# Optimization experiments

Measured on AMD Instinct MI355X. Metric: run time of the kernel, lower is better.

## Reference

```python
import jax, jax.numpy as jnp
import numpy as np

N_NODES = 50000
N_EDGES = 800000
D_FEAT = 128
D_EDGE = 64
N_HEADS = 4
OUT_DIM = 32
HID = N_HEADS * OUT_DIM  # 128


def segment_softmax(logits, seg, num_segments):
    # jraph.segment_softmax: subtract per-segment max, exp, normalize by per-segment sum
    seg_max = jax.ops.segment_max(logits, seg, num_segments=num_segments)
    e = jnp.exp(logits - seg_max[seg])
    denom = jax.ops.segment_sum(e, seg, num_segments=num_segments)
    return e / denom[seg]


def setup_inputs() -> dict:
    key = jax.random.key(0)
    ks = jax.random.split(key, 12)
    s = 1.0 / np.sqrt(D_FEAT)
    se = 1.0 / np.sqrt(D_EDGE)
    return {
        "nodes": jax.random.normal(ks[0], (N_NODES, D_FEAT), jnp.float32),
        "edges": jax.random.normal(ks[1], (N_EDGES, D_EDGE), jnp.float32),
        "senders": jax.random.randint(ks[2], (N_EDGES,), 0, N_NODES, jnp.int32),
        "receivers": jax.random.randint(ks[3], (N_EDGES,), 0, N_NODES, jnp.int32),
        "Wq": jax.random.normal(ks[4], (D_FEAT, HID), jnp.float32) * s,
        "bq": jnp.zeros((HID,), jnp.float32),
        "Wk": jax.random.normal(ks[5], (D_FEAT, HID), jnp.float32) * s,
        "bk": jnp.zeros((HID,), jnp.float32),
        "Wv": jax.random.normal(ks[6], (D_FEAT, HID), jnp.float32) * s,
        "bv": jnp.zeros((HID,), jnp.float32),
        "We": jax.random.normal(ks[7], (D_EDGE, HID), jnp.float32) * se,
        "Wu": jax.random.normal(ks[8], (D_FEAT, OUT_DIM), jnp.float32) * s,
        "bu": jnp.zeros((OUT_DIM,), jnp.float32),
    }


def reference(nodes, edges, senders, receivers, Wq, bq, Wk, bk, Wv, bv, We, Wu, bu):
    n_nodes = nodes.shape[0]
    send_feats = nodes[senders]    # [E, D]
    recv_feats = nodes[receivers]  # [E, D]

    q = (recv_feats @ Wq + bq).reshape(-1, N_HEADS, OUT_DIM)
    k = (send_feats @ Wk + bk).reshape(-1, N_HEADS, OUT_DIM)
    v = (send_feats @ Wv + bv).reshape(-1, N_HEADS, OUT_DIM)
    e = (edges @ We).reshape(-1, N_HEADS, OUT_DIM)

    attn = (q * k).sum(-1) / jnp.sqrt(jnp.asarray(OUT_DIM, q.dtype))  # [E, H]
    attn = segment_softmax(attn, receivers, n_nodes)                  # [E, H]

    msgs = (attn[:, :, None] * (v + e)).mean(axis=1)                  # [E, OUT_DIM]
    aggr = jax.ops.segment_sum(msgs, receivers, num_segments=n_nodes) # [N, OUT_DIM]

    feats = nodes @ Wu + bu
    return jax.nn.relu(feats + aggr)
```

## Files before the change

### kernel.cpp

```cpp
#include <hip/hip_runtime.h>
#include <math.h>

#define N_NODES 50000
#define N_EDGES 800000
#define D_FEAT 128
#define D_EDGE 64
#define HID 128
#define OUT_DIM 32

typedef unsigned short u16;
typedef short bf16x8 __attribute__((ext_vector_type(8)));
typedef float f32x4 __attribute__((ext_vector_type(4)));

__device__ __forceinline__ u16 f2bf(float x) {
    unsigned u = __float_as_uint(x);
    unsigned r = (u >> 16) & 1u;
    return (u16)((u + 0x7FFFu + r) >> 16);
}
__device__ __forceinline__ float bf2f(u16 s) { return __uint_as_float(((unsigned)s) << 16); }
__device__ __forceinline__ float bflo(unsigned u) { return __uint_as_float(u << 16); }
__device__ __forceinline__ float bfhi(unsigned u) { return __uint_as_float(u & 0xFFFF0000u); }

__global__ void zero_i32(int* __restrict__ p, int n) {
    int i = blockIdx.x * 256 + threadIdx.x;
    if (i < n) p[i] = 0;
}

__global__ void prep_WeT(const float* __restrict__ We, u16* __restrict__ WeTg) {
    int id = blockIdx.x * 256 + threadIdx.x;
    int c = id >> 6, k = id & 63;
    WeTg[c * 64 + k] = f2bf(We[k * HID + c]);
}

__global__ __launch_bounds__(256) void node_qkv_gemm2b(
    const float* __restrict__ nodes,
    const float* __restrict__ Wq, const float* __restrict__ bq,
    const float* __restrict__ Wk, const float* __restrict__ bk,
    const float* __restrict__ Wv, const float* __restrict__ bv,
    u16* __restrict__ Q, u16* __restrict__ Kk, u16* __restrict__ V)
{
    const int c0 = blockIdx.y * 64;
    const int n0 = blockIdx.x * 64;
    const float* Ws[3] = {Wq, Wk, Wv};
    const float* bs[3] = {bq, bk, bv};
    u16* Cs[3]         = {Q, Kk, V};

    __shared__ float Alds[32][68];
    __shared__ float Wlds[3][32][64];

    const int tid = threadIdx.x;
    const int tx = tid & 15, ty = tid >> 4;
    const int r = ty * 4, c = tx * 4;
    float acc[3][4][4] = {};

    for (int kk = 0; kk < D_FEAT; kk += 32) {
        #pragma unroll
        for (int it = 0; it < 2; ++it) {
            int idx = tid + it * 256;
            int an = idx >> 3;
            int ak = (idx & 7) * 4;
            float4 v4 = make_float4(0.f, 0.f, 0.f, 0.f);
            if (n0 + an < N_NODES)
                v4 = *(const float4*)&nodes[(size_t)(n0 + an) * D_FEAT + kk + ak];
            Alds[ak + 0][an] = v4.x;
            Alds[ak + 1][an] = v4.y;
            Alds[ak + 2][an] = v4.z;
            Alds[ak + 3][an] = v4.w;
        }
        #pragma unroll
        for (int it = 0; it < 6; ++it) {
            int idx = tid + it * 256;
            int m  = idx >> 9;
            int rm = idx & 511;
            int wk = rm >> 4;
            int wc = (rm & 15) * 4;
            *(float4*)&Wlds[m][wk][wc] = *(const float4*)&Ws[m][(size_t)(kk + wk) * HID + c0 + wc];
        }
        __syncthreads();
        #pragma unroll
        for (int k = 0; k < 32; ++k) {
            float4 a4 = *(const float4*)&Alds[k][r];
            float av[4] = {a4.x, a4.y, a4.z, a4.w};
            #pragma unroll
            for (int m = 0; m < 3; ++m) {
                float4 w4 = *(const float4*)&Wlds[m][k][c];
                float wv[4] = {w4.x, w4.y, w4.z, w4.w};
                #pragma unroll
                for (int i = 0; i < 4; ++i)
                    #pragma unroll
                    for (int j = 0; j < 4; ++j)
                        acc[m][i][j] += av[i] * wv[j];
            }
        }
        __syncthreads();
    }
    #pragma unroll
    for (int m = 0; m < 3; ++m) {
        #pragma unroll
        for (int i = 0; i < 4; ++i) {
            int n = n0 + r + i;
            if (n < N_NODES) {
                ushort4 o;
                o.x = f2bf(acc[m][i][0] + bs[m][c0 + c + 0]);
                o.y = f2bf(acc[m][i][1] + bs[m][c0 + c + 1]);
                o.z = f2bf(acc[m][i][2] + bs[m][c0 + c + 2]);
                o.w = f2bf(acc[m][i][3] + bs[m][c0 + c + 3]);
                *(ushort4*)&Cs[m][(size_t)n * HID + c0 + c] = o;
            }
        }
    }
}

__global__ void hist_kernel(const int* __restrict__ receivers, int* __restrict__ count) {
    int e = blockIdx.x * 256 + threadIdx.x;
    atomicAdd(&count[receivers[e]], 1);
}

__global__ __launch_bounds__(256) void scan1(const int* __restrict__ count,
                                             int* __restrict__ incl, int* __restrict__ bsum) {
    __shared__ int sh[256];
    int gid = blockIdx.x * 256 + threadIdx.x;
    int v = (gid < N_NODES) ? count[gid] : 0;
    sh[threadIdx.x] = v; __syncthreads();
    #pragma unroll
    for (int off = 1; off < 256; off <<= 1) {
        int t = (threadIdx.x >= off) ? sh[threadIdx.x - off] : 0;
        __syncthreads();
        sh[threadIdx.x] += t;
        __syncthreads();
    }
    if (gid < N_NODES) incl[gid] = sh[threadIdx.x];
    if (threadIdx.x == 255) bsum[blockIdx.x] = sh[255];
}

__global__ __launch_bounds__(256) void scan2(const int* __restrict__ bsum,
                                             int* __restrict__ boff, int nblocks) {
    __shared__ int sh[256];
    int v = (threadIdx.x < nblocks) ? bsum[threadIdx.x] : 0;
    sh[threadIdx.x] = v; __syncthreads();
    #pragma unroll
    for (int off = 1; off < 256; off <<= 1) {
        int t = (threadIdx.x >= off) ? sh[threadIdx.x - off] : 0;
        __syncthreads();
        sh[threadIdx.x] += t;
        __syncthreads();
    }
    boff[threadIdx.x] = sh[threadIdx.x] - v;
}

__global__ __launch_bounds__(256) void scan3(const int* __restrict__ incl,
                                             const int* __restrict__ count,
                                             const int* __restrict__ boff,
                                             int* __restrict__ startp, int* __restrict__ cursor) {
    int gid = blockIdx.x * 256 + threadIdx.x;
    if (gid < N_NODES) {
        int ex = incl[gid] - count[gid] + boff[blockIdx.x];
        startp[gid] = ex;
        cursor[gid] = ex;
    }
    if (gid == 0) startp[N_NODES] = N_EDGES;
}

__global__ void scatter_kernel(const int* __restrict__ receivers,
                               int* __restrict__ cursor, int* __restrict__ sorted,
                               int* __restrict__ epos) {
    int e = blockIdx.x * 256 + threadIdx.x;
    int r = receivers[e];
    int pos = atomicAdd(&cursor[r], 1);
    sorted[pos] = e;
    epos[e] = pos;
}

__global__ __launch_bounds__(256) void edge_logits_sorted_b(
    const u16* __restrict__ Q, const u16* __restrict__ K,
    const int* __restrict__ senders, const int* __restrict__ receivers,
    const int* __restrict__ sorted, float* __restrict__ wbuf)
{
    int id = blockIdx.x * 256 + threadIdx.x;
    int i = id >> 2, h = id & 3;
    int e = sorted[i];
    int s = senders[e], r = receivers[e];
    const uint4* qp = (const uint4*)&Q[(size_t)r * HID + h * 32];
    const uint4* kp = (const uint4*)&K[(size_t)s * HID + h * 32];
    float acc = 0.f;
    #pragma unroll
    for (int j = 0; j < 4; ++j) {
        uint4 a = qp[j], b = kp[j];
        acc += bflo(a.x) * bflo(b.x) + bfhi(a.x) * bfhi(b.x);
        acc += bflo(a.y) * bflo(b.y) + bfhi(a.y) * bfhi(b.y);
        acc += bflo(a.z) * bflo(b.z) + bfhi(a.z) * bfhi(b.z);
        acc += bflo(a.w) * bflo(b.w) + bfhi(a.w) * bfhi(b.w);
    }
    wbuf[id] = expf(acc * 0.17677669529663687f);
}

__global__ __launch_bounds__(256) void denom_norm(
    const int* __restrict__ startp, float* __restrict__ wbuf)
{
    int id = blockIdx.x * 256 + threadIdx.x;
    if (id >= N_NODES * 4) return;
    int n = id >> 2, h = id & 3;
    int s = startp[n], e = startp[n + 1];
    float acc = 0.f;
    for (int i = s; i < e; ++i)
        acc += wbuf[(size_t)i * 4 + h];
    float inv = 0.25f / acc;
    for (int i = s; i < e; ++i)
        wbuf[(size_t)i * 4 + h] *= inv;
}

__global__ __launch_bounds__(256, 2) void edge_messages_v5(
    const float* __restrict__ edges, const u16* __restrict__ WeTg,
    const u16* __restrict__ V, const float* __restrict__ wbuf,
    const int* __restrict__ senders, const int* __restrict__ epos,
    u16* __restrict__ msg)
{
    __shared__ __align__(16) u16 smem[18432];
    u16* Ae  = smem;
    u16* WeT = smem + 9216;
    u16* Ep  = smem;

    const int tid = threadIdx.x;
    const int e0 = blockIdx.x * 128;

    const int eloc = tid >> 1, half = tid & 1;
    const int eg = e0 + eloc;
    const int snd = senders[eg];
    const int pos = epos[eg];
    const float4 w4 = *(const float4*)&wbuf[(size_t)pos * 4];
    const float wA = half ? w4.z : w4.x;
    const float wB = half ? w4.w : w4.y;
    uint4 vv[8];
    {
        const uint4* vp = (const uint4*)&V[(size_t)snd * HID + half * 64];
        #pragma unroll
        for (int i = 0; i < 8; ++i) vv[i] = vp[i];
    }

    #pragma unroll
    for (int it = 0; it < 8; ++it) {
        int idx = tid + it * 256;
        int e  = idx >> 4;
        int k4 = (idx & 15) * 4;
        float4 v = *(const float4*)&edges[(size_t)(e0 + e) * D_EDGE + k4];
        ushort4 b;
        b.x = f2bf(v.x); b.y = f2bf(v.y); b.z = f2bf(v.z); b.w = f2bf(v.w);
        *(ushort4*)&Ae[e * 72 + k4] = b;
    }
    {
        int c = tid >> 1, part = tid & 1;
        const uint4* src = (const uint4*)&WeTg[c * 64 + part * 32];
        uint4* dst = (uint4*)&WeT[c * 72 + part * 32];
        dst[0] = src[0];
        dst[1] = src[1];
        dst[2] = src[2];
        dst[3] = src[3];
    }
    __syncthreads();

    const int wave = tid >> 6, lane = tid & 63;
    const int quad = lane >> 4, l15 = lane & 15;
    const int eb = wave * 32;

    bf16x8 afr[2][2];
    #pragma unroll
    for (int rt = 0; rt < 2; ++rt)
        #pragma unroll
        for (int ks = 0; ks < 2; ++ks)
            afr[rt][ks] = *(const bf16x8*)&Ae[(eb + rt * 16 + l15) * 72 + ks * 32 + quad * 8];

    f32x4 acc[2][8];
    #pragma unroll
    for (int rt = 0; rt < 2; ++rt)
        #pragma unroll
        for (int ct = 0; ct < 8; ++ct)
            acc[rt][ct] = (f32x4){0.f, 0.f, 0.f, 0.f};

    #pragma unroll
    for (int ct = 0; ct < 8; ++ct) {
        bf16x8 b0 = *(const bf16x8*)&WeT[(ct * 16 + l15) * 72 +  0 + quad * 8];
        bf16x8 b1 = *(const bf16x8*)&WeT[(ct * 16 + l15) * 72 + 32 + quad * 8];
        #pragma unroll
        for (int rt = 0; rt < 2; ++rt) {
            acc[rt][ct] = __builtin_amdgcn_mfma_f32_16x16x32_bf16(afr[rt][0], b0, acc[rt][ct], 0, 0, 0);
            acc[rt][ct] = __builtin_amdgcn_mfma_f32_16x16x32_bf16(afr[rt][1], b1, acc[rt][ct], 0, 0, 0);
        }
    }
    __syncthreads();

    #pragma unroll
    for (int rt = 0; rt < 2; ++rt)
        #pragma unroll
        for (int ct = 0; ct < 8; ++ct)
            #pragma unroll
            for (int r = 0; r < 4; ++r)
                Ep[(eb + rt * 16 + quad * 4 + r) * 136 + ct * 16 + l15] = f2bf(acc[rt][ct][r]);
    __syncthreads();

    uint4 ep4[8];
    {
        const uint4* epp = (const uint4*)&Ep[eloc * 136 + half * 64];
        #pragma unroll
        for (int i = 0; i < 8; ++i) ep4[i] = epp[i];
    }
    const unsigned* eu = (const unsigned*)ep4;
    const unsigned* vu = (const unsigned*)vv;

    float su[32];
    #pragma unroll
    for (int t = 0; t < 16; ++t) {
        unsigned ua = eu[t],      ub = eu[16 + t];
        unsigned va = vu[t],      vb = vu[16 + t];
        float p0 = wA * (bflo(ua) + bflo(va)) + wB * (bflo(ub) + bflo(vb));
        float p1 = wA * (bfhi(ua) + bfhi(va)) + wB * (bfhi(ub) + bfhi(vb));
        su[2 * t]     = p0 + __shfl_xor(p0, 1, 64);
        su[2 * t + 1] = p1 + __shfl_xor(p1, 1, 64);
    }
    unsigned ow[8];
    #pragma unroll
    for (int j = 0; j < 8; ++j) {
        int d0 = half * 16 + 2 * j;
        ow[j] = (unsigned)f2bf(su[d0]) | ((unsigned)f2bf(su[d0 + 1]) << 16);
    }
    uint4* mp = (uint4*)&msg[(size_t)pos * OUT_DIM + half * 16];
    mp[0] = make_uint4(ow[0], ow[1], ow[2], ow[3]);
    mp[1] = make_uint4(ow[4], ow[5], ow[6], ow[7]);
}

__global__ __launch_bounds__(256) void aggregate3(
    const u16* __restrict__ msg, const float* __restrict__ nodes,
    const float* __restrict__ Wu, const float* __restrict__ bu,
    const int* __restrict__ startp, float* __restrict__ out)
{
    int id = blockIdx.x * 256 + threadIdx.x;
    int n = id >> 5, d = id & 31;
    float acc = bu[d];
    #pragma unroll 4
    for (int i = 0; i < D_FEAT; ++i)
        acc += nodes[(size_t)n * D_FEAT + i] * Wu[i * OUT_DIM + d];
    int s = startp[n], e = startp[n + 1];
    for (int i = s; i < e; ++i)
        acc += bf2f(msg[(size_t)i * OUT_DIM + d]);
    out[id] = fmaxf(acc, 0.f);
}

extern "C" void kernel_launch(void* const* d_in, const int* in_sizes, int n_in,
                              void* d_out, int out_size, void* d_ws, size_t ws_size,
                              hipStream_t stream) {
    const float* nodes     = (const float*)d_in[0];
    const float* edges     = (const float*)d_in[1];
    const int*   senders   = (const int*)d_in[2];
    const int*   receivers = (const int*)d_in[3];
    const float* Wq = (const float*)d_in[4];
    const float* bq = (const float*)d_in[5];
    const float* Wk = (const float*)d_in[6];
    const float* bk = (const float*)d_in[7];
    const float* Wv = (const float*)d_in[8];
    const float* bv = (const float*)d_in[9];
    const float* We = (const float*)d_in[10];
    const float* Wu = (const float*)d_in[11];
    const float* bu = (const float*)d_in[12];
    float* out = (float*)d_out;

    char* p = (char*)d_ws;
    u16* Qb   = (u16*)p; p += (size_t)N_NODES * HID * 2;
    u16* Kb   = (u16*)p; p += (size_t)N_NODES * HID * 2;
    u16* Vb   = (u16*)p; p += (size_t)N_NODES * HID * 2;
    u16* WeTg = (u16*)p; p += (size_t)HID * D_EDGE * 2;
    float* wbuf = (float*)p; p += (size_t)N_EDGES * 4 * 4;
    u16* msg  = (u16*)p; p += (size_t)N_EDGES * OUT_DIM * 2;
    int* count  = (int*)p; p += (size_t)N_NODES * 4;
    int* incl   = (int*)p; p += (size_t)N_NODES * 4;
    int* startp = (int*)p; p += (size_t)(N_NODES + 4) * 4;
    int* cursor = (int*)p; p += (size_t)N_NODES * 4;
    int* sorted = (int*)p; p += (size_t)N_EDGES * 4;
    int* epos   = (int*)p; p += (size_t)N_EDGES * 4;
    int* bsum   = (int*)p; p += 256 * 4;
    int* boff   = (int*)p; p += 256 * 4;

    const int SCAN_BLOCKS = (N_NODES + 255) / 256;

    hipLaunchKernelGGL(zero_i32, dim3(SCAN_BLOCKS), dim3(256), 0, stream, count, N_NODES);
    hipLaunchKernelGGL(hist_kernel, dim3(N_EDGES / 256), dim3(256), 0, stream,
                       receivers, count);
    hipLaunchKernelGGL(scan1, dim3(SCAN_BLOCKS), dim3(256), 0, stream, count, incl, bsum);
    hipLaunchKernelGGL(scan2, dim3(1), dim3(256), 0, stream, bsum, boff, SCAN_BLOCKS);
    hipLaunchKernelGGL(scan3, dim3(SCAN_BLOCKS), dim3(256), 0, stream,
                       incl, count, boff, startp, cursor);
    hipLaunchKernelGGL(scatter_kernel, dim3(N_EDGES / 256), dim3(256), 0, stream,
                       receivers, cursor, sorted, epos);
    hipLaunchKernelGGL(prep_WeT, dim3(HID * D_EDGE / 256), dim3(256), 0, stream, We, WeTg);
    hipLaunchKernelGGL(node_qkv_gemm2b, dim3((N_NODES + 63) / 64, 2), dim3(256), 0, stream,
                       nodes, Wq, bq, Wk, bk, Wv, bv, Qb, Kb, Vb);
    hipLaunchKernelGGL(edge_logits_sorted_b, dim3(N_EDGES * 4 / 256), dim3(256), 0, stream,
                       Qb, Kb, senders, receivers, sorted, wbuf);
    hipLaunchKernelGGL(denom_norm, dim3((N_NODES * 4 + 255) / 256), dim3(256), 0, stream,
                       startp, wbuf);
    hipLaunchKernelGGL(edge_messages_v5, dim3(N_EDGES / 128), dim3(256), 0, stream,
                       edges, WeTg, Vb, wbuf, senders, epos, msg);
    hipLaunchKernelGGL(aggregate3, dim3(N_NODES * OUT_DIM / 256), dim3(256), 0, stream,
                       msg, nodes, Wu, bu, startp, out);
}
```

Measured before the change: 713.4 us.

## Use MFMA for QKV projection, permute V, restructure edge logits and messages

```diff
diff --git a/kernel.cpp b/kernel.cpp
--- a/kernel.cpp
+++ b/kernel.cpp
@@ -26,88 +26,90 @@
     if (i < n) p[i] = 0;
 }
 
-__global__ void prep_WeT(const float* __restrict__ We, u16* __restrict__ WeTg) {
+__global__ void prep_weights(const float* __restrict__ Wq, const float* __restrict__ Wk,
+                             const float* __restrict__ Wv, const float* __restrict__ We,
+                             u16* __restrict__ WT_all, u16* __restrict__ WeTg) {
     int id = blockIdx.x * 256 + threadIdx.x;
-    int c = id >> 6, k = id & 63;
-    WeTg[c * 64 + k] = f2bf(We[k * HID + c]);
-}
-
-__global__ __launch_bounds__(256) void node_qkv_gemm2b(
-    const float* __restrict__ nodes,
-    const float* __restrict__ Wq, const float* __restrict__ bq,
-    const float* __restrict__ Wk, const float* __restrict__ bk,
-    const float* __restrict__ Wv, const float* __restrict__ bv,
-    u16* __restrict__ Q, u16* __restrict__ Kk, u16* __restrict__ V)
-{
-    const int c0 = blockIdx.y * 64;
-    const int n0 = blockIdx.x * 64;
-    const float* Ws[3] = {Wq, Wk, Wv};
-    const float* bs[3] = {bq, bk, bv};
-    u16* Cs[3]         = {Q, Kk, V};
-
-    __shared__ float Alds[32][68];
-    __shared__ float Wlds[3][32][64];
+    if (id < 49152) {
+        int m = id >> 14, rem = id & 16383;
+        int c = rem >> 7, k = rem & 127;
+        const float* W = (m == 0) ? Wq : (m == 1) ? Wk : Wv;
+        WT_all[id] = f2bf(W[k * HID + c]);
+    } else {
+        int j = id - 49152;
+        int c = j >> 6, k = j & 63;
+        WeTg[j] = f2bf(We[k * HID + c]);
+    }
+}
+
+__global__ __launch_bounds__(256) void node_qkv_mfma(
+    const float* __restrict__ nodes, const u16* __restrict__ WT_all,
+    const float* __restrict__ bq, const float* __restrict__ bk, const float* __restrict__ bv,
+    u16* __restrict__ Q, u16* __restrict__ Kk, u16* __restrict__ Vp)
+{
+    const int mtile = blockIdx.y;
+    const int n0 = blockIdx.x * 128;
+    const u16* WT = WT_all + (size_t)mtile * 16384;
+    const float* bvec = (mtile == 0) ? bq : (mtile == 1) ? bk : bv;
+    u16* C = (mtile == 0) ? Q : (mtile == 1) ? Kk : Vp;
+
+    __shared__ __align__(16) u16 Alds[128 * 136];
 
     const int tid = threadIdx.x;
-    const int tx = tid & 15, ty = tid >> 4;
-    const int r = ty * 4, c = tx * 4;
-    float acc[3][4][4] = {};
-
-    for (int kk = 0; kk < D_FEAT; kk += 32) {
-        #pragma unroll
-        for (int it = 0; it < 2; ++it) {
-            int idx = tid + it * 256;
-            int an = idx >> 3;
-            int ak = (idx & 7) * 4;
-            float4 v4 = make_float4(0.f, 0.f, 0.f, 0.f);
-            if (n0 + an < N_NODES)
-                v4 = *(const float4*)&nodes[(size_t)(n0 + an) * D_FEAT + kk + ak];
-            Alds[ak + 0][an] = v4.x;
-            Alds[ak + 1][an] = v4.y;
-            Alds[ak + 2][an] = v4.z;
-            Alds[ak + 3][an] = v4.w;
+    #pragma unroll
+    for (int it = 0; it < 16; ++it) {
+        int idx = tid + it * 256;
+        int row = idx >> 5, k4 = (idx & 31) * 4;
+        float4 v = make_float4(0.f, 0.f, 0.f, 0.f);
+        if (n0 + row < N_NODES)
+            v = *(const float4*)&nodes[(size_t)(n0 + row) * D_FEAT + k4];
+        ushort4 b;
+        b.x = f2bf(v.x); b.y = f2bf(v.y); b.z = f2bf(v.z); b.w = f2bf(v.w);
+        *(ushort4*)&Alds[row * 136 + k4] = b;
+    }
+    __syncthreads();
+
+    const int wave = tid >> 6, lane = tid & 63;
+    const int quad = lane >> 4, l15 = lane & 15;
+    const int eb = wave * 32;
+
+    bf16x8 afr[2][4];
+    #pragma unroll
+    for (int rt = 0; rt < 2; ++rt)
+        #pragma unroll
+        for (int ks = 0; ks < 4; ++ks)
+            afr[rt][ks] = *(const bf16x8*)&Alds[(eb + rt * 16 + l15) * 136 + ks * 32 + quad * 8];
+
+    f32x4 acc[2][8];
+    #pragma unroll
+    for (int rt = 0; rt < 2; ++rt)
+        #pragma unroll
+        for (int ct = 0; ct < 8; ++ct)
+            acc[rt][ct] = (f32x4){0.f, 0.f, 0.f, 0.f};
+
+    #pragma unroll
+    for (int ks = 0; ks < 4; ++ks) {
+        #pragma unroll
+        for (int ct = 0; ct < 8; ++ct) {
+            bf16x8 b = *(const bf16x8*)&WT[(ct * 16 + l15) * 128 + ks * 32 + quad * 8];
+            acc[0][ct] = __builtin_amdgcn_mfma_f32_16x16x32_bf16(afr[0][ks], b, acc[0][ct], 0, 0, 0);
+            acc[1][ct] = __builtin_amdgcn_mfma_f32_16x16x32_bf16(afr[1][ks], b, acc[1][ct], 0, 0, 0);
         }
-        #pragma unroll
-        for (int it = 0; it < 6; ++it) {
-            int idx = tid + it * 256;
-            int m  = idx >> 9;
-            int rm = idx & 511;
-            int wk = rm >> 4;
-            int wc = (rm & 15) * 4;
-            *(float4*)&Wlds[m][wk][wc] = *(const float4*)&Ws[m][(size_t)(kk + wk) * HID + c0 + wc];
-        }
-        __syncthreads();
-        #pragma unroll
-        for (int k = 0; k < 32; ++k) {
-            float4 a4 = *(const float4*)&Alds[k][r];
-            float av[4] = {a4.x, a4.y, a4.z, a4.w};
+    }
+
+    #pragma unroll
+    for (int ct = 0; ct < 8; ++ct) {
+        int cbase = ct * 16 + l15;
+        float bias = bvec[cbase];
+        int oidx = (mtile == 2) ? ((cbase & 31) * 4 + (cbase >> 5)) : cbase;
+        #pragma unroll
+        for (int rt = 0; rt < 2; ++rt)
             #pragma unroll
-            for (int m = 0; m < 3; ++m) {
-                float4 w4 = *(const float4*)&Wlds[m][k][c];
-                float wv[4] = {w4.x, w4.y, w4.z, w4.w};
-                #pragma unroll
-                for (int i = 0; i < 4; ++i)
-                    #pragma unroll
-                    for (int j = 0; j < 4; ++j)
-                        acc[m][i][j] += av[i] * wv[j];
+            for (int r = 0; r < 4; ++r) {
+                int n = n0 + eb + rt * 16 + quad * 4 + r;
+                if (n < N_NODES)
+                    C[(size_t)n * HID + oidx] = f2bf(acc[rt][ct][r] + bias);
             }
-        }
-        __syncthreads();
-    }
-    #pragma unroll
-    for (int m = 0; m < 3; ++m) {
-        #pragma unroll
-        for (int i = 0; i < 4; ++i) {
-            int n = n0 + r + i;
-            if (n < N_NODES) {
-                ushort4 o;
-                o.x = f2bf(acc[m][i][0] + bs[m][c0 + c + 0]);
-                o.y = f2bf(acc[m][i][1] + bs[m][c0 + c + 1]);
-                o.z = f2bf(acc[m][i][2] + bs[m][c0 + c + 2]);
-                o.w = f2bf(acc[m][i][3] + bs[m][c0 + c + 3]);
-                *(ushort4*)&Cs[m][(size_t)n * HID + c0 + c] = o;
-            }
-        }
     }
 }
 
@@ -171,70 +173,85 @@
     epos[e] = pos;
 }
 
-__global__ __launch_bounds__(256) void edge_logits_sorted_b(
+__global__ __launch_bounds__(256) void edge_logits_v2(
     const u16* __restrict__ Q, const u16* __restrict__ K,
     const int* __restrict__ senders, const int* __restrict__ receivers,
     const int* __restrict__ sorted, float* __restrict__ wbuf)
 {
     int id = blockIdx.x * 256 + threadIdx.x;
-    int i = id >> 2, h = id & 3;
+    int i = id >> 1, half = id & 1;
     int e = sorted[i];
     int s = senders[e], r = receivers[e];
-    const uint4* qp = (const uint4*)&Q[(size_t)r * HID + h * 32];
-    const uint4* kp = (const uint4*)&K[(size_t)s * HID + h * 32];
-    float acc = 0.f;
+    const uint4* qp = (const uint4*)&Q[(size_t)r * HID + half * 64];
+    const uint4* kp = (const uint4*)&K[(size_t)s * HID + half * 64];
+    float a0 = 0.f, a1 = 0.f;
     #pragma unroll
     for (int j = 0; j < 4; ++j) {
         uint4 a = qp[j], b = kp[j];
-        acc += bflo(a.x) * bflo(b.x) + bfhi(a.x) * bfhi(b.x);
-        acc += bflo(a.y) * bflo(b.y) + bfhi(a.y) * bfhi(b.y);
-        acc += bflo(a.z) * bflo(b.z) + bfhi(a.z) * bfhi(b.z);
-        acc += bflo(a.w) * bflo(b.w) + bfhi(a.w) * bfhi(b.w);
-    }
-    wbuf[id] = expf(acc * 0.17677669529663687f);
-}
-
-__global__ __launch_bounds__(256) void denom_norm(
+        a0 += bflo(a.x) * bflo(b.x) + bfhi(a.x) * bfhi(b.x);
+        a0 += bflo(a.y) * bflo(b.y) + bfhi(a.y) * bfhi(b.y);
+        a0 += bflo(a.z) * bflo(b.z) + bfhi(a.z) * bfhi(b.z);
+        a0 += bflo(a.w) * bflo(b.w) + bfhi(a.w) * bfhi(b.w);
+    }
+    #pragma unroll
+    for (int j = 4; j < 8; ++j) {
+        uint4 a = qp[j], b = kp[j];
+        a1 += bflo(a.x) * bflo(b.x) + bfhi(a.x) * bfhi(b.x);
+        a1 += bflo(a.y) * bflo(b.y) + bfhi(a.y) * bfhi(b.y);
+        a1 += bflo(a.z) * bflo(b.z) + bfhi(a.z) * bfhi(b.z);
+        a1 += bflo(a.w) * bflo(b.w) + bfhi(a.w) * bfhi(b.w);
+    }
+    const float sc = 0.17677669529663687f;
+    float2 o = make_float2(expf(a0 * sc), expf(a1 * sc));
+    *(float2*)&wbuf[(size_t)i * 4 + half * 2] = o;
+}
+
+__global__ __launch_bounds__(256) void denom_norm2(
     const int* __restrict__ startp, float* __restrict__ wbuf)
 {
-    int id = blockIdx.x * 256 + threadIdx.x;
-    if (id >= N_NODES * 4) return;
-    int n = id >> 2, h = id & 3;
+    int n = blockIdx.x * 256 + threadIdx.x;
+    if (n >= N_NODES) return;
     int s = startp[n], e = startp[n + 1];
-    float acc = 0.f;
-    for (int i = s; i < e; ++i)
-        acc += wbuf[(size_t)i * 4 + h];
-    float inv = 0.25f / acc;
-    for (int i = s; i < e; ++i)
-        wbuf[(size_t)i * 4 + h] *= inv;
-}
-
-__global__ __launch_bounds__(256, 2) void edge_messages_v5(
+    float4 a = make_float4(0.f, 0.f, 0.f, 0.f);
+    for (int i = s; i < e; ++i) {
+        float4 w = *(const float4*)&wbuf[(size_t)i * 4];
+        a.x += w.x; a.y += w.y; a.z += w.z; a.w += w.w;
+    }
+    float4 inv;
+    inv.x = 0.25f / a.x; inv.y = 0.25f / a.y; inv.z = 0.25f / a.z; inv.w = 0.25f / a.w;
+    for (int i = s; i < e; ++i) {
+        float4 w = *(const float4*)&wbuf[(size_t)i * 4];
+        w.x *= inv.x; w.y *= inv.y; w.z *= inv.z; w.w *= inv.w;
+        *(float4*)&wbuf[(size_t)i * 4] = w;
+    }
+}
+
+__global__ __launch_bounds__(256) void edge_messages_v6(
     const float* __restrict__ edges, const u16* __restrict__ WeTg,
-    const u16* __restrict__ V, const float* __restrict__ wbuf,
+    const u16* __restrict__ Vp, const float* __restrict__ wbuf,
     const int* __restrict__ senders, const int* __restrict__ epos,
     u16* __restrict__ msg)
 {
-    __shared__ __align__(16) u16 smem[18432];
-    u16* Ae  = smem;
-    u16* WeT = smem + 9216;
-    u16* Ep  = smem;
+    __shared__ __align__(16) u16 Ae[128 * 72];
 
     const int tid = threadIdx.x;
     const int e0 = blockIdx.x * 128;
-
-    const int eloc = tid >> 1, half = tid & 1;
-    const int eg = e0 + eloc;
-    const int snd = senders[eg];
-    const int pos = epos[eg];
-    const float4 w4 = *(const float4*)&wbuf[(size_t)pos * 4];
-    const float wA = half ? w4.z : w4.x;
-    const float wB = half ? w4.w : w4.y;
-    uint4 vv[8];
-    {
-        const uint4* vp = (const uint4*)&V[(size_t)snd * HID + half * 64];
-        #pragma unroll
-        for (int i = 0; i < 8; ++i) vv[i] = vp[i];
+    const int wave = tid >> 6, lane = tid & 63;
+    const int quad = lane >> 4, l15 = lane & 15;
+    const int eb = wave * 32;
+
+    int snd8[8], pos8[8];
+    #pragma unroll
+    for (int idx = 0; idx < 8; ++idx) {
+        int el = e0 + eb + (idx >> 2) * 16 + quad * 4 + (idx & 3);
+        snd8[idx] = senders[el];
+        pos8[idx] = epos[el];
+    }
+    float w8[8][4];
+    #pragma unroll
+    for (int idx = 0; idx < 8; ++idx) {
+        float4 w = *(const float4*)&wbuf[(size_t)pos8[idx] * 4];
+        w8[idx][0] = w.x; w8[idx][1] = w.y; w8[idx][2] = w.z; w8[idx][3] = w.w;
     }
 
     #pragma unroll
@@ -247,20 +264,7 @@
         b.x = f2bf(v.x); b.y = f2bf(v.y); b.z = f2bf(v.z); b.w = f2bf(v.w);
         *(ushort4*)&Ae[e * 72 + k4] = b;
     }
-    {
-        int c = tid >> 1, part = tid & 1;
-        const uint4* src = (const uint4*)&WeTg[c * 64 + part * 32];
-        uint4* dst = (uint4*)&WeT[c * 72 + part * 32];
-        dst[0] = src[0];
-        dst[1] = src[1];
-        dst[2] = src[2];
-        dst[3] = src[3];
-    }
     __syncthreads();
-
-    const int wave = tid >> 6, lane = tid & 63;
-    const int quad = lane >> 4, l15 = lane & 15;
-    const int eb = wave * 32;
 
     bf16x8 afr[2][2];
     #pragma unroll
@@ -269,62 +273,41 @@
         for (int ks = 0; ks < 2; ++ks)
             afr[rt][ks] = *(const bf16x8*)&Ae[(eb + rt * 16 + l15) * 72 + ks * 32 + quad * 8];
 
-    f32x4 acc[2][8];
-    #pragma unroll
-    for (int rt = 0; rt < 2; ++rt)
-        #pragma unroll
-        for (int ct = 0; ct < 8; ++ct)
-            acc[rt][ct] = (f32x4){0.f, 0.f, 0.f, 0.f};
-
-    #pragma unroll
-    for (int ct = 0; ct < 8; ++ct) {
-        bf16x8 b0 = *(const bf16x8*)&WeT[(ct * 16 + l15) * 72 +  0 + quad * 8];
-        bf16x8 b1 = *(const bf16x8*)&WeT[(ct * 16 + l15) * 72 + 32 + quad * 8];
-        #pragma unroll
-        for (int rt = 0; rt < 2; ++rt) {
-            acc[rt][ct] = __builtin_amdgcn_mfma_f32_16x16x32_bf16(afr[rt][0], b0, acc[rt][ct], 0, 0, 0);
-            acc[rt][ct] = __builtin_amdgcn_mfma_f32_16x16x32_bf16(afr[rt][1], b1, acc[rt][ct], 0, 0, 0);
+    #pragma unroll
+    for (int p = 0; p < 2; ++p) {
+        const int d = p * 16 + l15;
+        ushort4 vp8[8];
+        #pragma unroll
+        for (int idx = 0; idx < 8; ++idx)
+            vp8[idx] = *(const ushort4*)&Vp[(size_t)snd8[idx] * HID + d * 4];
+
+        f32x4 acc[2][4];
+        #pragma unroll
+        for (int rt = 0; rt < 2; ++rt)
+            #pragma unroll
+            for (int c = 0; c < 4; ++c)
+                acc[rt][c] = (f32x4){0.f, 0.f, 0.f, 0.f};
+
+        #pragma unroll
+        for (int ks = 0; ks < 2; ++ks) {
+            #pragma unroll
+            for (int c = 0; c < 4; ++c) {
+                bf16x8 b = *(const bf16x8*)&WeTg[((2 * c + p) * 16 + l15) * 64 + ks * 32 + quad * 8];
+                acc[0][c] = __builtin_amdgcn_mfma_f32_16x16x32_bf16(afr[0][ks], b, acc[0][c], 0, 0, 0);
+                acc[1][c] = __builtin_amdgcn_mfma_f32_16x16x32_bf16(afr[1][ks], b, acc[1][c], 0, 0, 0);
+            }
         }
-    }
-    __syncthreads();
-
-    #pragma unroll
-    for (int rt = 0; rt < 2; ++rt)
-        #pragma unroll
-        for (int ct = 0; ct < 8; ++ct)
-            #pragma unroll
-            for (int r = 0; r < 4; ++r)
-                Ep[(eb + rt * 16 + quad * 4 + r) * 136 + ct * 16 + l15] = f2bf(acc[rt][ct][r]);
-    __syncthreads();
-
-    uint4 ep4[8];
-    {
-        const uint4* epp = (const uint4*)&Ep[eloc * 136 + half * 64];
-        #pragma unroll
-        for (int i = 0; i < 8; ++i) ep4[i] = epp[i];
-    }
-    const unsigned* eu = (const unsigned*)ep4;
-    const unsigned* vu = (const unsigned*)vv;
-
-    float su[32];
-    #pragma unroll
-    for (int t = 0; t < 16; ++t) {
-        unsigned ua = eu[t],      ub = eu[16 + t];
-        unsigned va = vu[t],      vb = vu[16 + t];
-        float p0 = wA * (bflo(ua) + bflo(va)) + wB * (bflo(ub) + bflo(vb));
-        float p1 = wA * (bfhi(ua) + bfhi(va)) + wB * (bfhi(ub) + bfhi(vb));
-        su[2 * t]     = p0 + __shfl_xor(p0, 1, 64);
-        su[2 * t + 1] = p1 + __shfl_xor(p1, 1, 64);
-    }
-    unsigned ow[8];
-    #pragma unroll
-    for (int j = 0; j < 8; ++j) {
-        int d0 = half * 16 + 2 * j;
-        ow[j] = (unsigned)f2bf(su[d0]) | ((unsigned)f2bf(su[d0 + 1]) << 16);
-    }
-    uint4* mp = (uint4*)&msg[(size_t)pos * OUT_DIM + half * 16];
-    mp[0] = make_uint4(ow[0], ow[1], ow[2], ow[3]);
-    mp[1] = make_uint4(ow[4], ow[5], ow[6], ow[7]);
+
+        #pragma unroll
+        for (int idx = 0; idx < 8; ++idx) {
+            int rt = idx >> 2, r = idx & 3;
+            float out = w8[idx][0] * (acc[rt][0][r] + bf2f(vp8[idx].x))
+                      + w8[idx][1] * (acc[rt][1][r] + bf2f(vp8[idx].y))
+                      + w8[idx][2] * (acc[rt][2][r] + bf2f(vp8[idx].z))
+                      + w8[idx][3] * (acc[rt][3][r] + bf2f(vp8[idx].w));
+            msg[(size_t)pos8[idx] * OUT_DIM + d] = f2bf(out);
+        }
+    }
 }
 
 __global__ __launch_bounds__(256) void aggregate3(
@@ -363,12 +346,13 @@
     float* out = (float*)d_out;
 
     char* p = (char*)d_ws;
-    u16* Qb   = (u16*)p; p += (size_t)N_NODES * HID * 2;
-    u16* Kb   = (u16*)p; p += (size_t)N_NODES * HID * 2;
-    u16* Vb   = (u16*)p; p += (size_t)N_NODES * HID * 2;
-    u16* WeTg = (u16*)p; p += (size_t)HID * D_EDGE * 2;
+    u16* Qb    = (u16*)p; p += (size_t)N_NODES * HID * 2;
+    u16* Kb    = (u16*)p; p += (size_t)N_NODES * HID * 2;
+    u16* Vperm = (u16*)p; p += (size_t)N_NODES * HID * 2;
+    u16* WT_all= (u16*)p; p += (size_t)3 * HID * HID * 2;
+    u16* WeTg  = (u16*)p; p += (size_t)HID * D_EDGE * 2;
     float* wbuf = (float*)p; p += (size_t)N_EDGES * 4 * 4;
-    u16* msg  = (u16*)p; p += (size_t)N_EDGES * OUT_DIM * 2;
+    u16* msg   = (u16*)p; p += (size_t)N_EDGES * OUT_DIM * 2;
     int* count  = (int*)p; p += (size_t)N_NODES * 4;
     int* incl   = (int*)p; p += (size_t)N_NODES * 4;
     int* startp = (int*)p; p += (size_t)(N_NODES + 4) * 4;
@@ -389,15 +373,16 @@
                        incl, count, boff, startp, cursor);
     hipLaunchKernelGGL(scatter_kernel, dim3(N_EDGES / 256), dim3(256), 0, stream,
                        receivers, cursor, sorted, epos);
-    hipLaunchKernelGGL(prep_WeT, dim3(HID * D_EDGE / 256), dim3(256), 0, stream, We, WeTg);
-    hipLaunchKernelGGL(node_qkv_gemm2b, dim3((N_NODES + 63) / 64, 2), dim3(256), 0, stream,
-                       nodes, Wq, bq, Wk, bk, Wv, bv, Qb, Kb, Vb);
-    hipLaunchKernelGGL(edge_logits_sorted_b, dim3(N_EDGES * 4 / 256), dim3(256), 0, stream,
+    hipLaunchKernelGGL(prep_weights, dim3(57344 / 256), dim3(256), 0, stream,
+                       Wq, Wk, Wv, We, WT_all, WeTg);
+    hipLaunchKernelGGL(node_qkv_mfma, dim3((N_NODES + 127) / 128, 3), dim3(256), 0, stream,
+                       nodes, WT_all, bq, bk, bv, Qb, Kb, Vperm);
+    hipLaunchKernelGGL(edge_logits_v2, dim3(N_EDGES * 2 / 256), dim3(256), 0, stream,
                        Qb, Kb, senders, receivers, sorted, wbuf);
-    hipLaunchKernelGGL(denom_norm, dim3((N_NODES * 4 + 255) / 256), dim3(256), 0, stream,
+    hipLaunchKernelGGL(denom_norm2, dim3(SCAN_BLOCKS), dim3(256), 0, stream,
                        startp, wbuf);
-    hipLaunchKernelGGL(edge_messages_v5, dim3(N_EDGES / 128), dim3(256), 0, stream,
-                       edges, WeTg, Vb, wbuf, senders, epos, msg);
+    hipLaunchKernelGGL(edge_messages_v6, dim3(N_EDGES / 128), dim3(256), 0, stream,
+                       edges, WeTg, Vperm, wbuf, senders, epos, msg);
     hipLaunchKernelGGL(aggregate3, dim3(N_NODES * OUT_DIM / 256), dim3(256), 0, stream,
                        msg, nodes, Wu, bu, startp, out);
 }
```

Measured after the change: 683.8 us. -4.1%, faster.
